# Kernel tuning notes

Measured on AMD Instinct MI355X. Metric: run time of the kernel, lower is better.

Reference implementation:

```python
import jax, jax.numpy as jnp
import numpy as np

HIDDEN = 1024
N_HEADS = 16
HEAD_DIM = HIDDEN // N_HEADS
B, S = 4, 2048


def setup_inputs() -> dict:
    key = jax.random.key(0)
    ks = jax.random.split(key, 11)
    init = lambda k, shape: jax.random.normal(k, shape, dtype=jnp.float32) * (1.0 / np.sqrt(shape[0]))
    return {
        "query": jax.random.normal(ks[0], (B, S, HIDDEN), dtype=jnp.float32),
        "key": jax.random.normal(ks[1], (B, S, HIDDEN), dtype=jnp.float32),
        "value": jax.random.normal(ks[2], (B, S, HIDDEN), dtype=jnp.float32),
        "Wq": init(ks[3], (HIDDEN, HIDDEN)), "bq": jnp.zeros((HIDDEN,), jnp.float32),
        "Wk": init(ks[4], (HIDDEN, HIDDEN)), "bk": jnp.zeros((HIDDEN,), jnp.float32),
        "Wv": init(ks[5], (HIDDEN, HIDDEN)), "bv": jnp.zeros((HIDDEN,), jnp.float32),
        "Wo": init(ks[6], (HIDDEN, HIDDEN)), "bo": jnp.zeros((HIDDEN,), jnp.float32),
    }


def reference(query, key, value, Wq, bq, Wk, bk, Wv, bv, Wo, bo):
    b, s, h = query.shape
    # QKV projections
    Q = query @ Wq + bq
    K = key @ Wk + bk
    V = value @ Wv + bv
    # split heads: [B, H, S, D]
    Q = Q.reshape(b, s, N_HEADS, HEAD_DIM).transpose(0, 2, 1, 3)
    K = K.reshape(b, s, N_HEADS, HEAD_DIM).transpose(0, 2, 1, 3)
    V = V.reshape(b, s, N_HEADS, HEAD_DIM).transpose(0, 2, 1, 3)
    scale = jnp.sqrt(jnp.asarray(HEAD_DIM, query.dtype))
    # scores: [B, H, S, S]
    scores = jnp.einsum("bhqd,bhkd->bhqk", Q, K) / scale
    attn = jax.nn.softmax(scores, axis=-1)
    out = jnp.einsum("bhqk,bhkd->bhqd", attn, V)
    out = out.transpose(0, 2, 1, 3).reshape(b, s, h)
    return out @ Wo + bo
```

## Files before the change

kernel.cpp:

```cpp
#include <hip/hip_runtime.h>
#include <hip/hip_bf16.h>

#define HID 1024
#define NH 16
#define HD 64
#define SEQ 2048
#define MTOT 8192
#define QSCALE 0.18033688011112042f

typedef __bf16 bf16x8 __attribute__((ext_vector_type(8)));
typedef float f32x4 __attribute__((ext_vector_type(4)));

static __device__ __forceinline__ float fast_exp2(float x) {
#if __has_builtin(__builtin_amdgcn_exp2f)
    return __builtin_amdgcn_exp2f(x);
#else
    return __expf(x * 0.6931471805599453f);
#endif
}

static __device__ __forceinline__ unsigned short bfbits(float f) {
    __bf16 b = (__bf16)f;
    return __builtin_bit_cast(unsigned short, b);
}

static __device__ __forceinline__ bf16x8 frag16(const unsigned short* p) {
    return __builtin_bit_cast(bf16x8, *(const uint4*)p);
}

__global__ void wt4_kernel(const float* __restrict__ W0, const float* __restrict__ W1,
                           const float* __restrict__ W2, const float* __restrict__ W3,
                           unsigned short* __restrict__ T0, unsigned short* __restrict__ T1,
                           unsigned short* __restrict__ T2, unsigned short* __restrict__ T3) {
    __shared__ float tile[32][33];
    const int z = blockIdx.z;
    const float* W = (z == 0) ? W0 : (z == 1) ? W1 : (z == 2) ? W2 : W3;
    unsigned short* Wt = (z == 0) ? T0 : (z == 1) ? T1 : (z == 2) ? T2 : T3;
    const int n0 = blockIdx.x * 32, k0 = blockIdx.y * 32;
    const int tx = threadIdx.x, ty = threadIdx.y;
#pragma unroll
    for (int i = 0; i < 4; ++i)
        tile[ty + i * 8][tx] = W[(size_t)(k0 + ty + i * 8) * HID + n0 + tx];
    __syncthreads();
#pragma unroll
    for (int i = 0; i < 4; ++i)
        Wt[(size_t)(n0 + ty + i * 8) * HID + k0 + tx] = bfbits(tile[tx][ty + i * 8]);
}

__global__ __launch_bounds__(256, 2) void qkv_kernel(
    const float* __restrict__ qin, const float* __restrict__ kin, const float* __restrict__ vin,
    const unsigned short* __restrict__ Wtq, const unsigned short* __restrict__ Wtk,
    const unsigned short* __restrict__ Wtv,
    const float* __restrict__ bq, const float* __restrict__ bk, const float* __restrict__ bv,
    unsigned short* __restrict__ Qb, unsigned short* __restrict__ Kb,
    unsigned short* __restrict__ Vtb) {
    __shared__ unsigned short smA[128][40];
    __shared__ unsigned short smB[128][40];
    const int tid = threadIdx.x;
    const int lane = tid & 63;
    const int wid = tid >> 6, wr = wid >> 1, wc = wid & 1;
    const int lr = lane & 15, lk = lane >> 4;

    const int z = blockIdx.x >> 9;
    const int bid = blockIdx.x & 511;
    const int m0 = (bid & 63) * 128, n0 = (bid >> 6) * 128;

    const float* A = (z == 0) ? qin : (z == 1) ? kin : vin;
    const unsigned short* Bt = (z == 0) ? Wtq : (z == 1) ? Wtk : Wtv;
    const float* bias = (z == 0) ? bq : (z == 1) ? bk : bv;
    const float sc = (z == 0) ? QSCALE : 1.0f;

    const int srow = tid >> 1, skh = (tid & 1) * 16;

    f32x4 acc[4][4] = {};

    for (int kt = 0; kt < HID / 32; ++kt) {
        const int k0 = kt * 32;
        __syncthreads();
        {
            const float* src = A + (size_t)(m0 + srow) * HID + k0 + skh;
            float4 a0 = *(const float4*)(src);
            float4 a1 = *(const float4*)(src + 4);
            float4 a2 = *(const float4*)(src + 8);
            float4 a3 = *(const float4*)(src + 12);
            union { __bf16 h[8]; uint4 v; } u0, u1;
            u0.h[0] = (__bf16)a0.x; u0.h[1] = (__bf16)a0.y; u0.h[2] = (__bf16)a0.z; u0.h[3] = (__bf16)a0.w;
            u0.h[4] = (__bf16)a1.x; u0.h[5] = (__bf16)a1.y; u0.h[6] = (__bf16)a1.z; u0.h[7] = (__bf16)a1.w;
            u1.h[0] = (__bf16)a2.x; u1.h[1] = (__bf16)a2.y; u1.h[2] = (__bf16)a2.z; u1.h[3] = (__bf16)a2.w;
            u1.h[4] = (__bf16)a3.x; u1.h[5] = (__bf16)a3.y; u1.h[6] = (__bf16)a3.z; u1.h[7] = (__bf16)a3.w;
            *(uint4*)&smA[srow][skh] = u0.v;
            *(uint4*)&smA[srow][skh + 8] = u1.v;
        }
        {
            const unsigned short* src = Bt + (size_t)(n0 + srow) * HID + k0 + skh;
            *(uint4*)&smB[srow][skh] = *(const uint4*)(src);
            *(uint4*)&smB[srow][skh + 8] = *(const uint4*)(src + 8);
        }
        __syncthreads();
        bf16x8 af[4], bfr[4];
#pragma unroll
        for (int m = 0; m < 4; ++m) af[m] = frag16(&smA[wr * 64 + m * 16 + lr][lk * 8]);
#pragma unroll
        for (int n = 0; n < 4; ++n) bfr[n] = frag16(&smB[wc * 64 + n * 16 + lr][lk * 8]);
#pragma unroll
        for (int m = 0; m < 4; ++m)
#pragma unroll
            for (int n = 0; n < 4; ++n)
                acc[m][n] = __builtin_amdgcn_mfma_f32_16x16x32_bf16(af[m], bfr[n], acc[m][n], 0, 0, 0);
    }

#pragma unroll
    for (int m = 0; m < 4; ++m) {
#pragma unroll
        for (int n = 0; n < 4; ++n) {
            const int col = n0 + wc * 64 + n * 16 + lr;
            const float bv = bias[col];
            const int row0 = m0 + wr * 64 + m * 16 + lk * 4;
            const int b = row0 >> 11, s0 = row0 & 2047;
            const int h = col >> 6, d = col & 63;
            if (z == 2) {
                unsigned short* dst = Vtb + ((((size_t)b * NH + h) * HD + d) * SEQ + s0);
                uint2 pk;
                pk.x = (unsigned)bfbits(acc[m][n][0] + bv) |
                       ((unsigned)bfbits(acc[m][n][1] + bv) << 16);
                pk.y = (unsigned)bfbits(acc[m][n][2] + bv) |
                       ((unsigned)bfbits(acc[m][n][3] + bv) << 16);
                *(uint2*)dst = pk;
            } else {
                unsigned short* dst = (z == 0) ? Qb : Kb;
#pragma unroll
                for (int j = 0; j < 4; ++j) {
                    const float v = (acc[m][n][j] + bv) * sc;
                    dst[((((size_t)b * NH + h) * SEQ + (s0 + j)) << 6) + d] = bfbits(v);
                }
            }
        }
    }
}

__global__ __launch_bounds__(256, 2) void oproj_kernel(
    const unsigned short* __restrict__ Av, const unsigned short* __restrict__ Bt,
    const float* __restrict__ bias, float* __restrict__ Cv) {
    __shared__ unsigned short smA[128][40];
    __shared__ unsigned short smB[128][40];
    const int tid = threadIdx.x;
    const int lane = tid & 63;
    const int wid = tid >> 6, wr = wid >> 1, wc = wid & 1;
    const int lr = lane & 15, lk = lane >> 4;
    const int m0 = blockIdx.x * 128, n0 = blockIdx.y * 128;
    const int srow = tid >> 1, skh = (tid & 1) * 16;

    f32x4 acc[4][4] = {};

    for (int kt = 0; kt < HID / 32; ++kt) {
        const int k0 = kt * 32;
        __syncthreads();
        {
            const unsigned short* src = Av + (size_t)(m0 + srow) * HID + k0 + skh;
            *(uint4*)&smA[srow][skh] = *(const uint4*)(src);
            *(uint4*)&smA[srow][skh + 8] = *(const uint4*)(src + 8);
        }
        {
            const unsigned short* src = Bt + (size_t)(n0 + srow) * HID + k0 + skh;
            *(uint4*)&smB[srow][skh] = *(const uint4*)(src);
            *(uint4*)&smB[srow][skh + 8] = *(const uint4*)(src + 8);
        }
        __syncthreads();
        bf16x8 af[4], bfr[4];
#pragma unroll
        for (int m = 0; m < 4; ++m) af[m] = frag16(&smA[wr * 64 + m * 16 + lr][lk * 8]);
#pragma unroll
        for (int n = 0; n < 4; ++n) bfr[n] = frag16(&smB[wc * 64 + n * 16 + lr][lk * 8]);
#pragma unroll
        for (int m = 0; m < 4; ++m)
#pragma unroll
            for (int n = 0; n < 4; ++n)
                acc[m][n] = __builtin_amdgcn_mfma_f32_16x16x32_bf16(af[m], bfr[n], acc[m][n], 0, 0, 0);
    }

#pragma unroll
    for (int m = 0; m < 4; ++m) {
#pragma unroll
        for (int n = 0; n < 4; ++n) {
            const int col = n0 + wc * 64 + n * 16 + lr;
            const float bv = bias[col];
#pragma unroll
            for (int j = 0; j < 4; ++j) {
                const int row = m0 + wr * 64 + m * 16 + lk * 4 + j;
                Cv[(size_t)row * HID + col] = acc[m][n][j] + bv;
            }
        }
    }
}

__global__ __launch_bounds__(512, 4) void flash_kernel(
    const unsigned short* __restrict__ Q, const unsigned short* __restrict__ K,
    const unsigned short* __restrict__ Vt, unsigned short* __restrict__ O) {
    __shared__ unsigned short smK[64][72];
    __shared__ unsigned short smV[64][72];
    __shared__ unsigned short smP[8][32][72];

    const int tid = threadIdx.x;
    const int lane = tid & 63, w = tid >> 6;
    const int lr = lane & 15, lk = lane >> 4;

    const int L = blockIdx.y * 8 + blockIdx.x;
    const int xcd = L & 7, slot = L >> 3;
    const int bh = xcd + 8 * (slot >> 3);
    const int qt = slot & 7;

    const int b = bh >> 4, h = bh & 15;
    const int q0 = qt * 256 + w * 32;

    const unsigned short* Qb = Q + (size_t)bh * SEQ * HD;
    const unsigned short* Kb = K + (size_t)bh * SEQ * HD;
    const unsigned short* Vb = Vt + (size_t)bh * HD * SEQ;

    bf16x8 qf[2][2];
#pragma unroll
    for (int m = 0; m < 2; ++m)
#pragma unroll
        for (int kk = 0; kk < 2; ++kk)
            qf[m][kk] = frag16(&Qb[(size_t)(q0 + m * 16 + lr) * HD + kk * 32 + lk * 8]);

    f32x4 accO[2][4] = {};
    float lsum[2] = {0.f, 0.f};

    const int srow = tid >> 3, sseg = (tid & 7) * 8;
    const unsigned short* Kp = Kb + (size_t)srow * HD + sseg;
    const unsigned short* Vp = Vb + (size_t)srow * SEQ + sseg;

    uint4 kr, vr;
    kr = *(const uint4*)Kp;
    vr = *(const uint4*)Vp;
    *(uint4*)&smK[srow][sseg] = kr;
    *(uint4*)&smV[srow][sseg] = vr;
    __syncthreads();

    const int NT = SEQ / 64;
    for (int kt = 0; kt < NT; ++kt) {
        if (kt + 1 < NT) {
            kr = *(const uint4*)(Kp + (size_t)(kt + 1) * 64 * HD);
            vr = *(const uint4*)(Vp + (kt + 1) * 64);
        }

        f32x4 s[2][4] = {};
#pragma unroll
        for (int kk = 0; kk < 2; ++kk) {
            bf16x8 kf[4];
#pragma unroll
            for (int n = 0; n < 4; ++n) kf[n] = frag16(&smK[n * 16 + lr][kk * 32 + lk * 8]);
#pragma unroll
            for (int m = 0; m < 2; ++m)
#pragma unroll
                for (int n = 0; n < 4; ++n)
                    s[m][n] = __builtin_amdgcn_mfma_f32_16x16x32_bf16(kf[n], qf[m][kk], s[m][n], 0, 0, 0);
        }

#pragma unroll
        for (int m = 0; m < 2; ++m) {
            float rs = 0.f;
#pragma unroll
            for (int n = 0; n < 4; ++n) {
                union { __bf16 hh[4]; uint2 v; } u;
#pragma unroll
                for (int j = 0; j < 4; ++j) {
                    const float p = fast_exp2(s[m][n][j]);
                    rs += p;
                    u.hh[j] = (__bf16)p;
                }
                *(uint2*)&smP[w][m * 16 + lr][n * 16 + lk * 4] = u.v;
            }
            lsum[m] += rs;
        }

#pragma unroll
        for (int ks = 0; ks < 2; ++ks) {
            bf16x8 pf[2], vf[4];
#pragma unroll
            for (int m = 0; m < 2; ++m) pf[m] = frag16(&smP[w][m * 16 + lr][ks * 32 + lk * 8]);
#pragma unroll
            for (int n = 0; n < 4; ++n) vf[n] = frag16(&smV[n * 16 + lr][ks * 32 + lk * 8]);
#pragma unroll
            for (int m = 0; m < 2; ++m)
#pragma unroll
                for (int n = 0; n < 4; ++n)
                    accO[m][n] = __builtin_amdgcn_mfma_f32_16x16x32_bf16(pf[m], vf[n], accO[m][n], 0, 0, 0);
        }
        __syncthreads();
        if (kt + 1 < NT) {
            *(uint4*)&smK[srow][sseg] = kr;
            *(uint4*)&smV[srow][sseg] = vr;
        }
        __syncthreads();
    }

#pragma unroll
    for (int m = 0; m < 2; ++m) {
        float t = lsum[m];
        t += __shfl_xor(t, 16);
        t += __shfl_xor(t, 32);
        const float invl = 1.0f / t;
#pragma unroll
        for (int j = 0; j < 4; ++j) {
            const float inv = __shfl(invl, lk * 4 + j);
            const int sg = q0 + m * 16 + lk * 4 + j;
#pragma unroll
            for (int n = 0; n < 4; ++n) {
                const int d = n * 16 + lr;
                O[((size_t)b * SEQ + sg) * HID + h * HD + d] = bfbits(accO[m][n][j] * inv);
            }
        }
    }
}

extern "C" void kernel_launch(void* const* d_in, const int* in_sizes, int n_in,
                              void* d_out, int out_size, void* d_ws, size_t ws_size,
                              hipStream_t stream) {
    const float* q  = (const float*)d_in[0];
    const float* k  = (const float*)d_in[1];
    const float* v  = (const float*)d_in[2];
    const float* Wq = (const float*)d_in[3]; const float* bq = (const float*)d_in[4];
    const float* Wk = (const float*)d_in[5]; const float* bk = (const float*)d_in[6];
    const float* Wv = (const float*)d_in[7]; const float* bv = (const float*)d_in[8];
    const float* Wo = (const float*)d_in[9]; const float* bo = (const float*)d_in[10];
    float* out = (float*)d_out;

    unsigned short* Wtq = (unsigned short*)d_ws;
    unsigned short* Wtk = Wtq + (size_t)HID * HID;
    unsigned short* Wtv = Wtk + (size_t)HID * HID;
    unsigned short* Wto = Wtv + (size_t)HID * HID;
    unsigned short* Qb  = Wto + (size_t)HID * HID;
    unsigned short* Kb  = Qb + (size_t)MTOT * HID;
    unsigned short* Vtb = Kb + (size_t)MTOT * HID;
    unsigned short* Ob  = Vtb + (size_t)MTOT * HID;

    wt4_kernel<<<dim3(32, 32, 4), dim3(32, 8), 0, stream>>>(
        Wq, Wk, Wv, Wo, Wtq, Wtk, Wtv, Wto);

    qkv_kernel<<<1536, 256, 0, stream>>>(q, k, v, Wtq, Wtk, Wtv, bq, bk, bv, Qb, Kb, Vtb);

    flash_kernel<<<dim3(8, 64), 512, 0, stream>>>(Qb, Kb, Vtb, Ob);

    oproj_kernel<<<dim3(64, 8), 256, 0, stream>>>(Ob, Wto, bo, out);
}
```

Measured before the change: 199.3 us.

## Use 32x32x16 MFMA in flash kernel and keep P in registers via permlane32 swap

The attention inner loop switches from 16x16x32 to 32x32x16 bf16 MFMA tiles, with each wave computing 32 queries against 64 keys. The exponentiated scores are packed to bf16 and rearranged across lane halves with v_permlane32_swap, so they feed the P·V MFMA directly as A operands. This removes the per-wave shared-memory round trip for P and its LDS traffic, and cuts the number of MFMA issues. In exchange it adds inline asm permutes and a shared-memory lookup for the row normalisation in the epilogue. It also relies on the fragment layout being exactly right for correctness.

```diff
diff --git a/kernel.cpp b/kernel.cpp
--- a/kernel.cpp
+++ b/kernel.cpp
@@ -10,6 +10,7 @@
 
 typedef __bf16 bf16x8 __attribute__((ext_vector_type(8)));
 typedef float f32x4 __attribute__((ext_vector_type(4)));
+typedef float f32x16 __attribute__((ext_vector_type(16)));
 
 static __device__ __forceinline__ float fast_exp2(float x) {
 #if __has_builtin(__builtin_amdgcn_exp2f)
@@ -22,6 +23,12 @@
 static __device__ __forceinline__ unsigned short bfbits(float f) {
     __bf16 b = (__bf16)f;
     return __builtin_bit_cast(unsigned short, b);
+}
+
+static __device__ __forceinline__ unsigned pk2(float lo, float hi) {
+    union { __bf16 h[2]; unsigned u; } v;
+    v.h[0] = (__bf16)lo; v.h[1] = (__bf16)hi;
+    return v.u;
 }
 
 static __device__ __forceinline__ bf16x8 frag16(const unsigned short* p) {
@@ -198,11 +205,11 @@
     const unsigned short* __restrict__ Vt, unsigned short* __restrict__ O) {
     __shared__ unsigned short smK[64][72];
     __shared__ unsigned short smV[64][72];
-    __shared__ unsigned short smP[8][32][72];
+    __shared__ float smL[8][32];
 
     const int tid = threadIdx.x;
     const int lane = tid & 63, w = tid >> 6;
-    const int lr = lane & 15, lk = lane >> 4;
+    const int l31 = lane & 31, hi = lane >> 5;
 
     const int L = blockIdx.y * 8 + blockIdx.x;
     const int xcd = L & 7, slot = L >> 3;
@@ -216,23 +223,20 @@
     const unsigned short* Kb = K + (size_t)bh * SEQ * HD;
     const unsigned short* Vb = Vt + (size_t)bh * HD * SEQ;
 
-    bf16x8 qf[2][2];
-#pragma unroll
-    for (int m = 0; m < 2; ++m)
-#pragma unroll
-        for (int kk = 0; kk < 2; ++kk)
-            qf[m][kk] = frag16(&Qb[(size_t)(q0 + m * 16 + lr) * HD + kk * 32 + lk * 8]);
-
-    f32x4 accO[2][4] = {};
-    float lsum[2] = {0.f, 0.f};
+    bf16x8 qf[4];
+#pragma unroll
+    for (int ks = 0; ks < 4; ++ks)
+        qf[ks] = frag16(&Qb[(size_t)(q0 + l31) * HD + ks * 16 + hi * 8]);
+
+    f32x16 accO[2] = {};
+    float lsum = 0.f;
 
     const int srow = tid >> 3, sseg = (tid & 7) * 8;
     const unsigned short* Kp = Kb + (size_t)srow * HD + sseg;
     const unsigned short* Vp = Vb + (size_t)srow * SEQ + sseg;
 
-    uint4 kr, vr;
-    kr = *(const uint4*)Kp;
-    vr = *(const uint4*)Vp;
+    uint4 kr = *(const uint4*)Kp;
+    uint4 vr = *(const uint4*)Vp;
     *(uint4*)&smK[srow][sseg] = kr;
     *(uint4*)&smV[srow][sseg] = vr;
     __syncthreads();
@@ -244,49 +248,49 @@
             vr = *(const uint4*)(Vp + (kt + 1) * 64);
         }
 
-        f32x4 s[2][4] = {};
-#pragma unroll
-        for (int kk = 0; kk < 2; ++kk) {
-            bf16x8 kf[4];
-#pragma unroll
-            for (int n = 0; n < 4; ++n) kf[n] = frag16(&smK[n * 16 + lr][kk * 32 + lk * 8]);
-#pragma unroll
-            for (int m = 0; m < 2; ++m)
-#pragma unroll
-                for (int n = 0; n < 4; ++n)
-                    s[m][n] = __builtin_amdgcn_mfma_f32_16x16x32_bf16(kf[n], qf[m][kk], s[m][n], 0, 0, 0);
-        }
-
-#pragma unroll
-        for (int m = 0; m < 2; ++m) {
-            float rs = 0.f;
-#pragma unroll
-            for (int n = 0; n < 4; ++n) {
-                union { __bf16 hh[4]; uint2 v; } u;
-#pragma unroll
-                for (int j = 0; j < 4; ++j) {
-                    const float p = fast_exp2(s[m][n][j]);
-                    rs += p;
-                    u.hh[j] = (__bf16)p;
-                }
-                *(uint2*)&smP[w][m * 16 + lr][n * 16 + lk * 4] = u.v;
-            }
-            lsum[m] += rs;
-        }
-
-#pragma unroll
-        for (int ks = 0; ks < 2; ++ks) {
-            bf16x8 pf[2], vf[4];
-#pragma unroll
-            for (int m = 0; m < 2; ++m) pf[m] = frag16(&smP[w][m * 16 + lr][ks * 32 + lk * 8]);
-#pragma unroll
-            for (int n = 0; n < 4; ++n) vf[n] = frag16(&smV[n * 16 + lr][ks * 32 + lk * 8]);
-#pragma unroll
-            for (int m = 0; m < 2; ++m)
-#pragma unroll
-                for (int n = 0; n < 4; ++n)
-                    accO[m][n] = __builtin_amdgcn_mfma_f32_16x16x32_bf16(pf[m], vf[n], accO[m][n], 0, 0, 0);
-        }
+        f32x16 s[2] = {};
+#pragma unroll
+        for (int t = 0; t < 2; ++t)
+#pragma unroll
+            for (int ks = 0; ks < 4; ++ks) {
+                bf16x8 kf = frag16(&smK[t * 32 + l31][ks * 16 + hi * 8]);
+                s[t] = __builtin_amdgcn_mfma_f32_32x32x16_bf16(kf, qf[ks], s[t], 0, 0, 0);
+            }
+
+        bf16x8 pa[4];
+        float rs = 0.f;
+#pragma unroll
+        for (int t = 0; t < 2; ++t) {
+            float p[16];
+#pragma unroll
+            for (int r = 0; r < 16; ++r) {
+                p[r] = fast_exp2(s[t][r]);
+                rs += p[r];
+            }
+#pragma unroll
+            for (int bb = 0; bb < 2; ++bb) {
+                const int R = bb * 8;
+                unsigned w0 = pk2(p[R + 0], p[R + 1]);
+                unsigned w1 = pk2(p[R + 2], p[R + 3]);
+                unsigned w2 = pk2(p[R + 4], p[R + 5]);
+                unsigned w3 = pk2(p[R + 6], p[R + 7]);
+                asm volatile("v_permlane32_swap_b32 %0, %1" : "+v"(w0), "+v"(w2));
+                asm volatile("v_permlane32_swap_b32 %0, %1" : "+v"(w1), "+v"(w3));
+                union { unsigned u[4]; bf16x8 v; } pu;
+                pu.u[0] = w0; pu.u[1] = w1; pu.u[2] = w2; pu.u[3] = w3;
+                pa[t * 2 + bb] = pu.v;
+            }
+        }
+        lsum += rs;
+
+#pragma unroll
+        for (int dt = 0; dt < 2; ++dt)
+#pragma unroll
+            for (int ks = 0; ks < 4; ++ks) {
+                bf16x8 vf = frag16(&smV[dt * 32 + l31][ks * 16 + hi * 8]);
+                accO[dt] = __builtin_amdgcn_mfma_f32_32x32x16_bf16(pa[ks], vf, accO[dt], 0, 0, 0);
+            }
+
         __syncthreads();
         if (kt + 1 < NT) {
             *(uint4*)&smK[srow][sseg] = kr;
@@ -295,23 +299,20 @@
         __syncthreads();
     }
 
-#pragma unroll
-    for (int m = 0; m < 2; ++m) {
-        float t = lsum[m];
-        t += __shfl_xor(t, 16);
-        t += __shfl_xor(t, 32);
-        const float invl = 1.0f / t;
-#pragma unroll
-        for (int j = 0; j < 4; ++j) {
-            const float inv = __shfl(invl, lk * 4 + j);
-            const int sg = q0 + m * 16 + lk * 4 + j;
-#pragma unroll
-            for (int n = 0; n < 4; ++n) {
-                const int d = n * 16 + lr;
-                O[((size_t)b * SEQ + sg) * HID + h * HD + d] = bfbits(accO[m][n][j] * inv);
-            }
-        }
-    }
+    lsum += __shfl_xor(lsum, 32);
+    smL[w][l31] = 1.0f / lsum;
+    __syncthreads();
+
+#pragma unroll
+    for (int dt = 0; dt < 2; ++dt)
+#pragma unroll
+        for (int r = 0; r < 16; ++r) {
+            const int row = (r & 3) + 8 * (r >> 2) + 4 * hi;
+            const float inv = smL[w][row];
+            const int sg = q0 + row;
+            O[((size_t)b * SEQ + sg) * HID + h * HD + dt * 32 + l31] =
+                bfbits(accO[dt][r] * inv);
+        }
 }
 
 extern "C" void kernel_launch(void* const* d_in, const int* in_sizes, int n_in,
```

After: 202.8 us. No clear change (+1.8%).
